# Optimization experiments

Measured on AMD Instinct MI355X. Metric: run time of the kernel, lower is better.

Reference implementation:

```python
import jax, jax.numpy as jnp
import numpy as np

DIM_IN = 512
DIM_OUT = 64


def setup_inputs() -> dict:
    key = jax.random.key(0)
    kx, kq, kk, kv = jax.random.split(key, 4)
    x = jax.random.normal(kx, (4, 4096, DIM_IN), dtype=jnp.float32)
    s = 1.0 / np.sqrt(DIM_IN)
    # torch nn.Linear stores weight as [out, in]; keep same convention
    Wq = jax.random.uniform(kq, (DIM_OUT, DIM_IN), jnp.float32, -s, s)
    Wk = jax.random.uniform(kk, (DIM_OUT, DIM_IN), jnp.float32, -s, s)
    Wv = jax.random.uniform(kv, (DIM_OUT, DIM_IN), jnp.float32, -s, s)
    return {"x": x, "Wq": Wq, "Wk": Wk, "Wv": Wv}


def reference(x, Wq, Wk, Wv):
    # q/k/v projections: [B,S,Din] @ [Din,Dout] -> [B,S,Dout]
    q = jnp.einsum("bsd,od->bso", x, Wq)
    k = jnp.einsum("bsd,od->bso", x, Wk)
    v = jnp.einsum("bsd,od->bso", x, Wv)
    scale = 1.0 / jnp.sqrt(jnp.asarray(q.shape[-1], q.dtype))
    scores = jnp.einsum("bqo,bko->bqk", q, k) * scale  # [B,S,S]
    weights = jax.nn.softmax(scores, axis=-1)
    out = jnp.einsum("bqk,bko->bqo", weights, v)  # [B,S,Dout]
    return out
```

## Files before the change

### kernel.cpp

```cpp
#include <hip/hip_runtime.h>
#include <hip/hip_bf16.h>

#define SEQ 4096
#define MTOT 16384

typedef float f32x4  __attribute__((ext_vector_type(4)));
typedef float f32x16 __attribute__((ext_vector_type(16)));
typedef _Float16 f16;
typedef _Float16 f16x4 __attribute__((ext_vector_type(4)));
typedef _Float16 f16x8 __attribute__((ext_vector_type(8)));
typedef unsigned int   u32;
typedef unsigned int   u32x2 __attribute__((ext_vector_type(2)));
typedef unsigned short u16;

static constexpr size_t QL_B   = 0;
static constexpr size_t KL_B   = 2u << 20;
static constexpr size_t VL_B   = 4u << 20;
static constexpr size_t WL_B   = 6u << 20;

__device__ __forceinline__ u16 h16(float v) { return __builtin_bit_cast(u16, (f16)v); }
__device__ __forceinline__ u32 pkrtz(float a, float b) {
  return __builtin_bit_cast(u32, __builtin_amdgcn_cvt_pkrtz(a, b));
}
__device__ __forceinline__ float ex2(float x) { return __builtin_amdgcn_exp2f(x); }
__device__ __forceinline__ void gl16(const u16* g, u16* l) {
  __builtin_amdgcn_global_load_lds((const __attribute__((address_space(1))) void*)g,
                                   (__attribute__((address_space(3))) void*)l, 16, 0, 0);
}

__global__ __launch_bounds__(256) void wconv_kernel(const float* __restrict__ Wq,
                                                    const float* __restrict__ Wk,
                                                    const float* __restrict__ Wv,
                                                    u16* __restrict__ wlin) {
  const float QSC = 0.18033688011112042f;
  int e = blockIdx.x * 256 + threadIdx.x;
  int flat = e * 4;
  int colg = flat >> 9;
  int k0   = flat & 511;
  int mat  = colg >> 6;
  const float* W = (mat == 0) ? Wq : (mat == 1 ? Wk : Wv);
  f32x4 v = *(const f32x4*)(W + (size_t)(colg & 63) * 512 + k0);
  if (mat == 0) v *= QSC;
  int s = colg >> 4, r16 = colg & 15;
  int step = k0 >> 5, g = (k0 & 31) >> 3, jb = k0 & 7;
  __attribute__((aligned(8))) u16 b[4];
#pragma unroll
  for (int j = 0; j < 4; ++j) b[j] = h16(v[j]);
  *(uint2*)(wlin + ((size_t)(s * 16 + step) * 64 + g * 16 + r16) * 8 + jb) = *(uint2*)b;
}

__global__ __launch_bounds__(256, 4) void proj_kernel(const float* __restrict__ x,
                                                      const u16* __restrict__ wlin,
                                                      u16* __restrict__ ws) {
  __shared__ __attribute__((aligned(16))) u16 xl[8192];
  float* scr = (float*)xl;

  const int tid  = threadIdx.x;
  const int blk  = blockIdx.x;
  const int lane = tid & 63;
  const int ng   = tid >> 6;
  const int r16  = lane & 15;
  const int g    = lane >> 4;
  const int m0   = blk * 16;

#pragma unroll
  for (int i = 0; i < 8; ++i) {
    int f = tid * 4 + i * 1024;
    int row = f >> 9, k0 = f & 511;
    f32x4 v = *(const f32x4*)(x + (size_t)m0 * 512 + f);
    __attribute__((aligned(8))) u16 b[4];
#pragma unroll
    for (int j = 0; j < 4; ++j) b[j] = h16(v[j]);
    int ln = ((k0 & 31) >> 3) * 16 + row;
    *(uint2*)(xl + ((size_t)(k0 >> 5) * 64 + ln) * 8 + (k0 & 7)) = *(uint2*)b;
  }
  __syncthreads();

  f32x4 acc[3];
#pragma unroll
  for (int s = 0; s < 3; ++s) acc[s] = (f32x4){0.f, 0.f, 0.f, 0.f};

#pragma unroll 2
  for (int step = 0; step < 16; ++step) {
    f16x8 a = *(const f16x8*)(xl + ((size_t)step * 64 + lane) * 8);
#pragma unroll
    for (int s = 0; s < 3; ++s) {
      int sg = ng * 3 + s;
      f16x8 b = *(const f16x8*)(wlin + ((size_t)(sg * 16 + step) * 64 + lane) * 8);
      acc[s] = __builtin_amdgcn_mfma_f32_16x16x32_f16(a, b, acc[s], 0, 0, 0);
    }
  }
  __syncthreads();

#pragma unroll
  for (int s = 0; s < 3; ++s)
#pragma unroll
    for (int rr = 0; rr < 4; ++rr)
      scr[(g * 4 + rr) * 193 + ng * 48 + s * 16 + r16] = acc[s][rr];
  __syncthreads();

  u16* Ql = ws + (QL_B >> 1);
  u16* Kl = ws + (KL_B >> 1);
  u16* Vl = ws + (VL_B >> 1);
  const int batch = m0 >> 12;
  const int tile  = (m0 >> 5) & 127;
  const int half  = (m0 >> 4) & 1;

  {
    int t2 = tid & 127;
    int r  = t2 & 15, hh = (t2 >> 4) & 1, ch = t2 >> 5;
    int l31 = half * 16 + r;
    __attribute__((aligned(16))) u16 b[8];
    if (tid < 128) {
#pragma unroll
      for (int j = 0; j < 8; ++j) b[j] = h16(scr[r * 193 + 64 + ch * 16 + hh * 8 + j]);
      *(uint4*)(Kl + ((size_t)((batch * 128 + tile) * 4 + ch) * 64 + hh * 32 + l31) * 8) =
          *(uint4*)b;
    } else {
#pragma unroll
      for (int j = 0; j < 8; ++j) b[j] = h16(scr[r * 193 + ch * 16 + hh * 8 + j]);
      int qhalf = (m0 >> 5);
      *(uint4*)(Ql + ((size_t)(qhalf * 4 + ch) * 64 + hh * 32 + l31) * 8) = *(uint4*)b;
    }
  }
  {
    int z = tid & 1, l31 = (tid >> 1) & 31, hh = (tid >> 6) & 1, db = tid >> 7;
    int d = db * 32 + l31;
    __attribute__((aligned(8))) u16 b[4];
#pragma unroll
    for (int j = 0; j < 4; ++j) b[j] = h16(scr[(8 * z + 4 * hh + j) * 193 + 128 + d]);
    *(uint2*)(Vl + ((size_t)(((batch * 128 + tile) * 2 + db) * 2 + half) * 64 + hh * 32 + l31) *
                       8 + z * 4) = *(uint2*)b;
  }
}

__global__ __launch_bounds__(256, 2) void attn_kernel(const u16* __restrict__ ws,
                                                      float* __restrict__ out) {
  __shared__ __attribute__((aligned(16))) u16 kvb[4][2][4096];

  const int tid  = threadIdx.x;
  const int w    = tid >> 6;
  const int lane = tid & 63;
  const int l31  = lane & 31;
  const int h    = lane >> 5;
  const int bx   = blockIdx.x;
  const int qb   = (bx & 7) * 64 + (bx >> 3);
  const int bb   = qb >> 7;

  const u16* Ql = ws + (QL_B >> 1);
  const u16* Kl = ws + (KL_B >> 1);
  const u16* Vl = ws + (VL_B >> 1);

  f16x8 qf[4];
#pragma unroll
  for (int ch = 0; ch < 4; ++ch)
    qf[ch] = *(const f16x8*)(Ql + ((size_t)(qb * 4 + ch) * 64 + lane) * 8);

  f32x16 oacc[2];
#pragma unroll
  for (int db = 0; db < 2; ++db)
#pragma unroll
    for (int r = 0; r < 16; ++r) oacc[db][r] = 0.f;
  float mrun = -INFINITY, lrun = 0.f;
  const float RTHR = 11.0f;

  const int t0 = bb * 128 + w * 32;
  u16* b0 = &kvb[w][0][0];
  u16* b1 = &kvb[w][1][0];

  auto stage = [&](u16* buf, int t) {
    const u16* ks = Kl + (size_t)t * 2048;
    const u16* vs = Vl + (size_t)t * 2048;
#pragma unroll
    for (int c = 0; c < 4; ++c) gl16(ks + c * 512 + lane * 8, buf + c * 512);
#pragma unroll
    for (int c = 0; c < 4; ++c) gl16(vs + c * 512 + lane * 8, buf + 2048 + c * 512);
  };

  stage(b0, t0);

#pragma unroll 1
  for (int it = 0; it < 32; ++it) {
    u16* cb = (it & 1) ? b1 : b0;
    u16* nb = (it & 1) ? b0 : b1;
    if (it < 31) {
      stage(nb, t0 + it + 1);
      asm volatile("s_waitcnt vmcnt(8)" ::: "memory");
    } else {
      asm volatile("s_waitcnt vmcnt(0)" ::: "memory");
    }
    __builtin_amdgcn_sched_barrier(0);

    f16x8 ka[4], vp[2][2];
#pragma unroll
    for (int ch = 0; ch < 4; ++ch)
      ka[ch] = *(const f16x8*)(cb + (ch * 64 + lane) * 8);
#pragma unroll
    for (int db = 0; db < 2; ++db)
#pragma unroll
      for (int pp = 0; pp < 2; ++pp)
        vp[db][pp] = *(const f16x8*)(cb + 2048 + ((db * 2 + pp) * 64 + lane) * 8);

    f32x16 sac;
#pragma unroll
    for (int r = 0; r < 16; ++r) sac[r] = 0.f;
#pragma unroll
    for (int ch = 0; ch < 4; ++ch)
      sac = __builtin_amdgcn_mfma_f32_32x32x16_f16(ka[ch], qf[ch], sac, 0, 0, 0);

    float mt = sac[0];
#pragma unroll
    for (int r = 1; r < 16; ++r) mt = fmaxf(mt, sac[r]);
    if (__any(mt > mrun + RTHR)) {
      float mtw  = fmaxf(mt, __shfl_xor(mt, 32));
      float nm   = fmaxf(mrun, mtw);
      float corr = ex2(mrun - nm);
      lrun *= corr;
      mrun = nm;
#pragma unroll
      for (int db = 0; db < 2; ++db)
#pragma unroll
        for (int r = 0; r < 16; ++r) oacc[db][r] *= corr;
    }
#pragma unroll
    for (int r = 0; r < 16; ++r) {
      float pv = ex2(sac[r] - mrun);
      sac[r] = pv;
      lrun += pv;
    }

    f16x4 pb[4];
#pragma unroll
    for (int c = 0; c < 4; ++c) {
      u32x2 pk;
      pk[0] = pkrtz(sac[4 * c + 0], sac[4 * c + 1]);
      pk[1] = pkrtz(sac[4 * c + 2], sac[4 * c + 3]);
      pb[c] = __builtin_bit_cast(f16x4, pk);
    }

#pragma unroll
    for (int db = 0; db < 2; ++db)
#pragma unroll
      for (int pp = 0; pp < 2; ++pp) {
        f16x4 vlo = __builtin_shufflevector(vp[db][pp], vp[db][pp], 0, 1, 2, 3);
        f16x4 vhi = __builtin_shufflevector(vp[db][pp], vp[db][pp], 4, 5, 6, 7);
        oacc[db] = __builtin_amdgcn_mfma_f32_32x32x8f16(vlo, pb[2 * pp], oacc[db], 0, 0, 0);
        oacc[db] = __builtin_amdgcn_mfma_f32_32x32x8f16(vhi, pb[2 * pp + 1], oacc[db], 0, 0, 0);
      }
  }

  lrun += __shfl_xor(lrun, 32);

  __syncthreads();
  float* po  = (float*)&kvb[0][0][0];
  float* mls = (float*)((char*)&kvb[0][0][0] + 35840);
  if (h == 0) {
    mls[(w * 32 + l31) * 2 + 0] = mrun;
    mls[(w * 32 + l31) * 2 + 1] = lrun;
  }
  __syncthreads();

  float mg = -INFINITY;
#pragma unroll
  for (int ww = 0; ww < 4; ++ww) mg = fmaxf(mg, mls[(ww * 32 + l31) * 2]);
  float wgt = ex2(mrun - mg);
#pragma unroll
  for (int db = 0; db < 2; ++db)
#pragma unroll
    for (int g = 0; g < 4; ++g) {
      f32x4 v = {oacc[db][4 * g + 0] * wgt, oacc[db][4 * g + 1] * wgt,
                 oacc[db][4 * g + 2] * wgt, oacc[db][4 * g + 3] * wgt};
      *(f32x4*)(po + (size_t)(w * 32 + l31) * 68 + db * 32 + 8 * g + 4 * h) = v;
    }
  __syncthreads();

#pragma unroll
  for (int i = 0; i < 2; ++i) {
    int idx = tid + i * 256;
    int q = idx >> 4, c4 = (idx & 15) * 4;
    float m2 = -INFINITY;
#pragma unroll
    for (int ww = 0; ww < 4; ++ww) m2 = fmaxf(m2, mls[(ww * 32 + q) * 2]);
    float l2 = 0.f;
#pragma unroll
    for (int ww = 0; ww < 4; ++ww)
      l2 += mls[(ww * 32 + q) * 2 + 1] * ex2(mls[(ww * 32 + q) * 2] - m2);
    f32x4 s = (f32x4){0.f, 0.f, 0.f, 0.f};
#pragma unroll
    for (int ww = 0; ww < 4; ++ww) s += *(const f32x4*)(po + (size_t)(ww * 32 + q) * 68 + c4);
    s *= (1.f / l2);
    *(f32x4*)(out + (size_t)(qb * 32 + q) * 64 + c4) = s;
  }
}

extern "C" void kernel_launch(void* const* d_in, const int* in_sizes, int n_in,
                              void* d_out, int out_size, void* d_ws, size_t ws_size,
                              hipStream_t stream) {
  const float* x  = (const float*)d_in[0];
  const float* Wq = (const float*)d_in[1];
  const float* Wk = (const float*)d_in[2];
  const float* Wv = (const float*)d_in[3];
  u16* ws = (u16*)d_ws;
  (void)in_sizes; (void)n_in; (void)out_size; (void)ws_size;

  wconv_kernel<<<96, 256, 0, stream>>>(Wq, Wk, Wv, ws + (WL_B >> 1));
  proj_kernel<<<1024, 256, 0, stream>>>(x, ws + (WL_B >> 1), ws);
  attn_kernel<<<512, 256, 0, stream>>>(ws, (float*)d_out);
}
```

Baseline: 55.03 us.

## Use 512-thread blocks with two query groups; load V directly to registers

Attention blocks grow to 8 waves covering two 32-row query groups that share the same key-split assignment, and the grid halves to 256 blocks. Only K is staged through LDS via async loads; V tiles are now loaded straight from global memory into registers with double buffering. The row max and row sum use tree reductions instead of serial chains. The aim is to cut LDS traffic and footprint and to shorten dependency chains, at the cost of more vector registers and a serialized two-pass final reduction with extra barriers.

```diff
diff --git a/kernel.cpp b/kernel.cpp
--- a/kernel.cpp
+++ b/kernel.cpp
@@ -134,18 +134,20 @@
   }
 }
 
-__global__ __launch_bounds__(256, 2) void attn_kernel(const u16* __restrict__ ws,
+__global__ __launch_bounds__(512, 2) void attn_kernel(const u16* __restrict__ ws,
                                                       float* __restrict__ out) {
-  __shared__ __attribute__((aligned(16))) u16 kvb[4][2][4096];
+  __shared__ __attribute__((aligned(16))) u16 kb[8][2][2048];
 
   const int tid  = threadIdx.x;
   const int w    = tid >> 6;
   const int lane = tid & 63;
   const int l31  = lane & 31;
   const int h    = lane >> 5;
+  const int qg   = w >> 2;
+  const int kq   = w & 3;
   const int bx   = blockIdx.x;
-  const int qb   = (bx & 7) * 64 + (bx >> 3);
-  const int bb   = qb >> 7;
+  const int qb   = (bx & 7) * 32 + (bx >> 3);
+  const int bb   = qb >> 6;
 
   const u16* Ql = ws + (QL_B >> 1);
   const u16* Kl = ws + (KL_B >> 1);
@@ -154,7 +156,7 @@
   f16x8 qf[4];
 #pragma unroll
   for (int ch = 0; ch < 4; ++ch)
-    qf[ch] = *(const f16x8*)(Ql + ((size_t)(qb * 4 + ch) * 64 + lane) * 8);
+    qf[ch] = *(const f16x8*)(Ql + ((size_t)((qb * 2 + qg) * 4 + ch) * 64 + lane) * 8);
 
   f32x16 oacc[2];
 #pragma unroll
@@ -164,42 +166,37 @@
   float mrun = -INFINITY, lrun = 0.f;
   const float RTHR = 11.0f;
 
-  const int t0 = bb * 128 + w * 32;
-  u16* b0 = &kvb[w][0][0];
-  u16* b1 = &kvb[w][1][0];
-
-  auto stage = [&](u16* buf, int t) {
+  const int t0 = bb * 128 + kq * 32;
+  u16* b0 = &kb[w][0][0];
+  u16* b1 = &kb[w][1][0];
+
+  auto stageK = [&](u16* buf, int t) {
     const u16* ks = Kl + (size_t)t * 2048;
-    const u16* vs = Vl + (size_t)t * 2048;
 #pragma unroll
     for (int c = 0; c < 4; ++c) gl16(ks + c * 512 + lane * 8, buf + c * 512);
-#pragma unroll
-    for (int c = 0; c < 4; ++c) gl16(vs + c * 512 + lane * 8, buf + 2048 + c * 512);
   };
-
-  stage(b0, t0);
-
-#pragma unroll 1
-  for (int it = 0; it < 32; ++it) {
-    u16* cb = (it & 1) ? b1 : b0;
-    u16* nb = (it & 1) ? b0 : b1;
-    if (it < 31) {
-      stage(nb, t0 + it + 1);
+  f16x8 v0[2][2], v1[2][2];
+  auto loadV = [&](f16x8(&vv)[2][2], int t) {
+#pragma unroll
+    for (int db = 0; db < 2; ++db)
+#pragma unroll
+      for (int pp = 0; pp < 2; ++pp)
+        vv[db][pp] = *(const f16x8*)(Vl + (size_t)t * 2048 + ((db * 2 + pp) * 64 + lane) * 8);
+  };
+
+  auto body = [&](u16* cb, u16* nb, f16x8(&vc)[2][2], f16x8(&vn)[2][2], int t, bool last) {
+    if (!last) {
+      stageK(nb, t + 1);
+      loadV(vn, t + 1);
       asm volatile("s_waitcnt vmcnt(8)" ::: "memory");
     } else {
       asm volatile("s_waitcnt vmcnt(0)" ::: "memory");
     }
     __builtin_amdgcn_sched_barrier(0);
 
-    f16x8 ka[4], vp[2][2];
-#pragma unroll
-    for (int ch = 0; ch < 4; ++ch)
-      ka[ch] = *(const f16x8*)(cb + (ch * 64 + lane) * 8);
-#pragma unroll
-    for (int db = 0; db < 2; ++db)
-#pragma unroll
-      for (int pp = 0; pp < 2; ++pp)
-        vp[db][pp] = *(const f16x8*)(cb + 2048 + ((db * 2 + pp) * 64 + lane) * 8);
+    f16x8 ka[4];
+#pragma unroll
+    for (int ch = 0; ch < 4; ++ch) ka[ch] = *(const f16x8*)(cb + (ch * 64 + lane) * 8);
 
     f32x16 sac;
 #pragma unroll
@@ -208,9 +205,12 @@
     for (int ch = 0; ch < 4; ++ch)
       sac = __builtin_amdgcn_mfma_f32_32x32x16_f16(ka[ch], qf[ch], sac, 0, 0, 0);
 
-    float mt = sac[0];
-#pragma unroll
-    for (int r = 1; r < 16; ++r) mt = fmaxf(mt, sac[r]);
+    float t8[8];
+#pragma unroll
+    for (int r = 0; r < 8; ++r) t8[r] = fmaxf(sac[2 * r], sac[2 * r + 1]);
+    float t4a = fmaxf(t8[0], t8[1]), t4b = fmaxf(t8[2], t8[3]);
+    float t4c = fmaxf(t8[4], t8[5]), t4d = fmaxf(t8[6], t8[7]);
+    float mt = fmaxf(fmaxf(t4a, t4b), fmaxf(t4c, t4d));
     if (__any(mt > mrun + RTHR)) {
       float mtw  = fmaxf(mt, __shfl_xor(mt, 32));
       float nm   = fmaxf(mrun, mtw);
@@ -223,11 +223,12 @@
         for (int r = 0; r < 16; ++r) oacc[db][r] *= corr;
     }
 #pragma unroll
-    for (int r = 0; r < 16; ++r) {
-      float pv = ex2(sac[r] - mrun);
-      sac[r] = pv;
-      lrun += pv;
-    }
+    for (int r = 0; r < 16; ++r) sac[r] = ex2(sac[r] - mrun);
+    float s4[4];
+#pragma unroll
+    for (int r = 0; r < 4; ++r)
+      s4[r] = (sac[4 * r] + sac[4 * r + 1]) + (sac[4 * r + 2] + sac[4 * r + 3]);
+    lrun += (s4[0] + s4[1]) + (s4[2] + s4[3]);
 
     f16x4 pb[4];
 #pragma unroll
@@ -242,54 +243,65 @@
     for (int db = 0; db < 2; ++db)
 #pragma unroll
       for (int pp = 0; pp < 2; ++pp) {
-        f16x4 vlo = __builtin_shufflevector(vp[db][pp], vp[db][pp], 0, 1, 2, 3);
-        f16x4 vhi = __builtin_shufflevector(vp[db][pp], vp[db][pp], 4, 5, 6, 7);
+        f16x4 vlo = __builtin_shufflevector(vc[db][pp], vc[db][pp], 0, 1, 2, 3);
+        f16x4 vhi = __builtin_shufflevector(vc[db][pp], vc[db][pp], 4, 5, 6, 7);
         oacc[db] = __builtin_amdgcn_mfma_f32_32x32x8f16(vlo, pb[2 * pp], oacc[db], 0, 0, 0);
         oacc[db] = __builtin_amdgcn_mfma_f32_32x32x8f16(vhi, pb[2 * pp + 1], oacc[db], 0, 0, 0);
       }
+  };
+
+  stageK(b0, t0);
+  loadV(v0, t0);
+#pragma unroll 1
+  for (int p = 0; p < 16; ++p) {
+    body(b0, b1, v0, v1, t0 + 2 * p, false);
+    body(b1, b0, v1, v0, t0 + 2 * p + 1, p == 15);
   }
 
   lrun += __shfl_xor(lrun, 32);
 
   __syncthreads();
-  float* po  = (float*)&kvb[0][0][0];
-  float* mls = (float*)((char*)&kvb[0][0][0] + 35840);
+  float* po  = (float*)&kb[0][0][0];
+  float* mls = (float*)((char*)&kb[0][0][0] + 36864);
   if (h == 0) {
     mls[(w * 32 + l31) * 2 + 0] = mrun;
     mls[(w * 32 + l31) * 2 + 1] = lrun;
   }
   __syncthreads();
 
-  float mg = -INFINITY;
-#pragma unroll
-  for (int ww = 0; ww < 4; ++ww) mg = fmaxf(mg, mls[(ww * 32 + l31) * 2]);
-  float wgt = ex2(mrun - mg);
-#pragma unroll
-  for (int db = 0; db < 2; ++db)
-#pragma unroll
-    for (int g = 0; g < 4; ++g) {
-      f32x4 v = {oacc[db][4 * g + 0] * wgt, oacc[db][4 * g + 1] * wgt,
-                 oacc[db][4 * g + 2] * wgt, oacc[db][4 * g + 3] * wgt};
-      *(f32x4*)(po + (size_t)(w * 32 + l31) * 68 + db * 32 + 8 * g + 4 * h) = v;
-    }
-  __syncthreads();
-
-#pragma unroll
-  for (int i = 0; i < 2; ++i) {
-    int idx = tid + i * 256;
-    int q = idx >> 4, c4 = (idx & 15) * 4;
-    float m2 = -INFINITY;
-#pragma unroll
-    for (int ww = 0; ww < 4; ++ww) m2 = fmaxf(m2, mls[(ww * 32 + q) * 2]);
-    float l2 = 0.f;
-#pragma unroll
-    for (int ww = 0; ww < 4; ++ww)
-      l2 += mls[(ww * 32 + q) * 2 + 1] * ex2(mls[(ww * 32 + q) * 2] - m2);
-    f32x4 s = (f32x4){0.f, 0.f, 0.f, 0.f};
-#pragma unroll
-    for (int ww = 0; ww < 4; ++ww) s += *(const f32x4*)(po + (size_t)(ww * 32 + q) * 68 + c4);
-    s *= (1.f / l2);
-    *(f32x4*)(out + (size_t)(qb * 32 + q) * 64 + c4) = s;
+#pragma unroll 1
+  for (int g = 0; g < 2; ++g) {
+    if (qg == g) {
+      float mg = -INFINITY;
+#pragma unroll
+      for (int k2 = 0; k2 < 4; ++k2) mg = fmaxf(mg, mls[((g * 4 + k2) * 32 + l31) * 2]);
+      float wgt = ex2(mrun - mg);
+#pragma unroll
+      for (int db = 0; db < 2; ++db)
+#pragma unroll
+        for (int gg = 0; gg < 4; ++gg) {
+          f32x4 v = {oacc[db][4 * gg + 0] * wgt, oacc[db][4 * gg + 1] * wgt,
+                     oacc[db][4 * gg + 2] * wgt, oacc[db][4 * gg + 3] * wgt};
+          *(f32x4*)(po + (size_t)(kq * 32 + l31) * 68 + db * 32 + 8 * gg + 4 * h) = v;
+        }
+    }
+    __syncthreads();
+    {
+      int q = tid >> 4, c4 = (tid & 15) * 4;
+      float m2 = -INFINITY;
+#pragma unroll
+      for (int k2 = 0; k2 < 4; ++k2) m2 = fmaxf(m2, mls[((g * 4 + k2) * 32 + q) * 2]);
+      float l2 = 0.f;
+#pragma unroll
+      for (int k2 = 0; k2 < 4; ++k2)
+        l2 += mls[((g * 4 + k2) * 32 + q) * 2 + 1] * ex2(mls[((g * 4 + k2) * 32 + q) * 2] - m2);
+      f32x4 s = (f32x4){0.f, 0.f, 0.f, 0.f};
+#pragma unroll
+      for (int k2 = 0; k2 < 4; ++k2) s += *(const f32x4*)(po + (size_t)(k2 * 32 + q) * 68 + c4);
+      s *= (1.f / l2);
+      *(f32x4*)(out + (size_t)(qb * 64 + g * 32 + q) * 64 + c4) = s;
+    }
+    __syncthreads();
   }
 }
 
@@ -305,5 +317,5 @@
 
   wconv_kernel<<<96, 256, 0, stream>>>(Wq, Wk, Wv, ws + (WL_B >> 1));
   proj_kernel<<<1024, 256, 0, stream>>>(x, ws + (WL_B >> 1), ws);
-  attn_kernel<<<512, 256, 0, stream>>>(ws, (float*)d_out);
-}
+  attn_kernel<<<256, 512, 0, stream>>>(ws, (float*)d_out);
+}
```

New measurement: 54.50 us, median of 3. About the same (-1.0%).

## Process two K/V tiles per iteration, load V to registers, sum rows via MFMA

Applied to the files above, without the earlier changes.

The attention loop now handles two 32-key tiles per iteration. Only K is staged into LDS, while V tiles are prefetched straight into registers and double-buffered. The softmax row sum is now computed by an MFMA against a ones vector, replacing the scalar VALU adds and the cross-half shuffle. This aims to cut per-iteration overhead, LDS traffic and VALU work, at the cost of many more VGPRs, which could hurt occupancy at two waves per SIMD. The scratch offset for the final reduction moves to match the new layout.

```diff
diff --git a/kernel.cpp b/kernel.cpp
--- a/kernel.cpp
+++ b/kernel.cpp
@@ -136,7 +136,7 @@
 
 __global__ __launch_bounds__(256, 2) void attn_kernel(const u16* __restrict__ ws,
                                                       float* __restrict__ out) {
-  __shared__ __attribute__((aligned(16))) u16 kvb[4][2][4096];
+  __shared__ __attribute__((aligned(16))) u16 kb[4][2][4096];
 
   const int tid  = threadIdx.x;
   const int w    = tid >> 6;
@@ -156,104 +156,139 @@
   for (int ch = 0; ch < 4; ++ch)
     qf[ch] = *(const f16x8*)(Ql + ((size_t)(qb * 4 + ch) * 64 + lane) * 8);
 
-  f32x16 oacc[2];
+  f32x16 oacc[2], lacc;
 #pragma unroll
   for (int db = 0; db < 2; ++db)
 #pragma unroll
     for (int r = 0; r < 16; ++r) oacc[db][r] = 0.f;
-  float mrun = -INFINITY, lrun = 0.f;
+#pragma unroll
+  for (int r = 0; r < 16; ++r) lacc[r] = 0.f;
+  float mrun = -INFINITY;
   const float RTHR = 11.0f;
+  const f16x4 ones = {(f16)1.f, (f16)1.f, (f16)1.f, (f16)1.f};
 
   const int t0 = bb * 128 + w * 32;
-  u16* b0 = &kvb[w][0][0];
-  u16* b1 = &kvb[w][1][0];
-
-  auto stage = [&](u16* buf, int t) {
-    const u16* ks = Kl + (size_t)t * 2048;
-    const u16* vs = Vl + (size_t)t * 2048;
-#pragma unroll
-    for (int c = 0; c < 4; ++c) gl16(ks + c * 512 + lane * 8, buf + c * 512);
-#pragma unroll
-    for (int c = 0; c < 4; ++c) gl16(vs + c * 512 + lane * 8, buf + 2048 + c * 512);
+  u16* b0 = &kb[w][0][0];
+  u16* b1 = &kb[w][1][0];
+
+  auto stageK = [&](u16* buf, int t) {
+#pragma unroll
+    for (int u = 0; u < 2; ++u)
+#pragma unroll
+      for (int c = 0; c < 4; ++c)
+        gl16(Kl + (size_t)(t + u) * 2048 + c * 512 + lane * 8, buf + u * 2048 + c * 512);
   };
-
-  stage(b0, t0);
-
-#pragma unroll 1
-  for (int it = 0; it < 32; ++it) {
-    u16* cb = (it & 1) ? b1 : b0;
-    u16* nb = (it & 1) ? b0 : b1;
-    if (it < 31) {
-      stage(nb, t0 + it + 1);
-      asm volatile("s_waitcnt vmcnt(8)" ::: "memory");
+  f16x8 vA[2][2][2], vB[2][2][2];
+  auto loadV = [&](f16x8(&vv)[2][2][2], int t) {
+#pragma unroll
+    for (int u = 0; u < 2; ++u)
+#pragma unroll
+      for (int db = 0; db < 2; ++db)
+#pragma unroll
+        for (int pp = 0; pp < 2; ++pp)
+          vv[u][db][pp] =
+              *(const f16x8*)(Vl + (size_t)(t + u) * 2048 + ((db * 2 + pp) * 64 + lane) * 8);
+  };
+
+  auto body = [&](u16* cb, u16* nb, f16x8(&vc)[2][2][2], f16x8(&vn)[2][2][2], int t,
+                  bool last) {
+    if (!last) {
+      stageK(nb, t + 2);
+      loadV(vn, t + 2);
+      asm volatile("s_waitcnt vmcnt(16)" ::: "memory");
     } else {
       asm volatile("s_waitcnt vmcnt(0)" ::: "memory");
     }
     __builtin_amdgcn_sched_barrier(0);
 
-    f16x8 ka[4], vp[2][2];
+    f32x16 sac0, sac1;
+#pragma unroll
+    for (int r = 0; r < 16; ++r) { sac0[r] = 0.f; sac1[r] = 0.f; }
+    f16x8 ka0[4], ka1[4];
+#pragma unroll
+    for (int ch = 0; ch < 4; ++ch) ka0[ch] = *(const f16x8*)(cb + (ch * 64 + lane) * 8);
 #pragma unroll
     for (int ch = 0; ch < 4; ++ch)
-      ka[ch] = *(const f16x8*)(cb + (ch * 64 + lane) * 8);
-#pragma unroll
-    for (int db = 0; db < 2; ++db)
-#pragma unroll
-      for (int pp = 0; pp < 2; ++pp)
-        vp[db][pp] = *(const f16x8*)(cb + 2048 + ((db * 2 + pp) * 64 + lane) * 8);
-
-    f32x16 sac;
-#pragma unroll
-    for (int r = 0; r < 16; ++r) sac[r] = 0.f;
+      ka1[ch] = *(const f16x8*)(cb + 2048 + (ch * 64 + lane) * 8);
 #pragma unroll
     for (int ch = 0; ch < 4; ++ch)
-      sac = __builtin_amdgcn_mfma_f32_32x32x16_f16(ka[ch], qf[ch], sac, 0, 0, 0);
-
-    float mt = sac[0];
-#pragma unroll
-    for (int r = 1; r < 16; ++r) mt = fmaxf(mt, sac[r]);
+      sac0 = __builtin_amdgcn_mfma_f32_32x32x16_f16(ka0[ch], qf[ch], sac0, 0, 0, 0);
+#pragma unroll
+    for (int ch = 0; ch < 4; ++ch)
+      sac1 = __builtin_amdgcn_mfma_f32_32x32x16_f16(ka1[ch], qf[ch], sac1, 0, 0, 0);
+
+    float t16[16];
+#pragma unroll
+    for (int r = 0; r < 16; ++r) t16[r] = fmaxf(sac0[r], sac1[r]);
+#pragma unroll
+    for (int r = 0; r < 8; ++r) t16[r] = fmaxf(t16[r], t16[r + 8]);
+#pragma unroll
+    for (int r = 0; r < 4; ++r) t16[r] = fmaxf(t16[r], t16[r + 4]);
+    float mt = fmaxf(fmaxf(t16[0], t16[1]), fmaxf(t16[2], t16[3]));
     if (__any(mt > mrun + RTHR)) {
       float mtw  = fmaxf(mt, __shfl_xor(mt, 32));
       float nm   = fmaxf(mrun, mtw);
       float corr = ex2(mrun - nm);
-      lrun *= corr;
       mrun = nm;
 #pragma unroll
       for (int db = 0; db < 2; ++db)
 #pragma unroll
         for (int r = 0; r < 16; ++r) oacc[db][r] *= corr;
-    }
-#pragma unroll
-    for (int r = 0; r < 16; ++r) {
-      float pv = ex2(sac[r] - mrun);
-      sac[r] = pv;
-      lrun += pv;
-    }
-
-    f16x4 pb[4];
+#pragma unroll
+      for (int r = 0; r < 16; ++r) lacc[r] *= corr;
+    }
+#pragma unroll
+    for (int r = 0; r < 16; ++r) sac0[r] = ex2(sac0[r] - mrun);
+#pragma unroll
+    for (int r = 0; r < 16; ++r) sac1[r] = ex2(sac1[r] - mrun);
+
+    f16x4 pb0[4], pb1[4];
 #pragma unroll
     for (int c = 0; c < 4; ++c) {
-      u32x2 pk;
-      pk[0] = pkrtz(sac[4 * c + 0], sac[4 * c + 1]);
-      pk[1] = pkrtz(sac[4 * c + 2], sac[4 * c + 3]);
-      pb[c] = __builtin_bit_cast(f16x4, pk);
-    }
+      u32x2 k0, k1;
+      k0[0] = pkrtz(sac0[4 * c + 0], sac0[4 * c + 1]);
+      k0[1] = pkrtz(sac0[4 * c + 2], sac0[4 * c + 3]);
+      k1[0] = pkrtz(sac1[4 * c + 0], sac1[4 * c + 1]);
+      k1[1] = pkrtz(sac1[4 * c + 2], sac1[4 * c + 3]);
+      pb0[c] = __builtin_bit_cast(f16x4, k0);
+      pb1[c] = __builtin_bit_cast(f16x4, k1);
+    }
+
+#pragma unroll
+    for (int c = 0; c < 4; ++c)
+      lacc = __builtin_amdgcn_mfma_f32_32x32x8f16(ones, pb0[c], lacc, 0, 0, 0);
+#pragma unroll
+    for (int c = 0; c < 4; ++c)
+      lacc = __builtin_amdgcn_mfma_f32_32x32x8f16(ones, pb1[c], lacc, 0, 0, 0);
 
 #pragma unroll
     for (int db = 0; db < 2; ++db)
 #pragma unroll
       for (int pp = 0; pp < 2; ++pp) {
-        f16x4 vlo = __builtin_shufflevector(vp[db][pp], vp[db][pp], 0, 1, 2, 3);
-        f16x4 vhi = __builtin_shufflevector(vp[db][pp], vp[db][pp], 4, 5, 6, 7);
-        oacc[db] = __builtin_amdgcn_mfma_f32_32x32x8f16(vlo, pb[2 * pp], oacc[db], 0, 0, 0);
-        oacc[db] = __builtin_amdgcn_mfma_f32_32x32x8f16(vhi, pb[2 * pp + 1], oacc[db], 0, 0, 0);
+        f16x4 vlo0 = __builtin_shufflevector(vc[0][db][pp], vc[0][db][pp], 0, 1, 2, 3);
+        f16x4 vhi0 = __builtin_shufflevector(vc[0][db][pp], vc[0][db][pp], 4, 5, 6, 7);
+        oacc[db] = __builtin_amdgcn_mfma_f32_32x32x8f16(vlo0, pb0[2 * pp], oacc[db], 0, 0, 0);
+        oacc[db] = __builtin_amdgcn_mfma_f32_32x32x8f16(vhi0, pb0[2 * pp + 1], oacc[db], 0, 0, 0);
+        f16x4 vlo1 = __builtin_shufflevector(vc[1][db][pp], vc[1][db][pp], 0, 1, 2, 3);
+        f16x4 vhi1 = __builtin_shufflevector(vc[1][db][pp], vc[1][db][pp], 4, 5, 6, 7);
+        oacc[db] = __builtin_amdgcn_mfma_f32_32x32x8f16(vlo1, pb1[2 * pp], oacc[db], 0, 0, 0);
+        oacc[db] = __builtin_amdgcn_mfma_f32_32x32x8f16(vhi1, pb1[2 * pp + 1], oacc[db], 0, 0, 0);
       }
-  }
-
-  lrun += __shfl_xor(lrun, 32);
-
-  __syncthreads();
-  float* po  = (float*)&kvb[0][0][0];
-  float* mls = (float*)((char*)&kvb[0][0][0] + 35840);
+  };
+
+  stageK(b0, t0);
+  loadV(vA, t0);
+#pragma unroll 1
+  for (int p = 0; p < 8; ++p) {
+    body(b0, b1, vA, vB, t0 + 4 * p, false);
+    body(b1, b0, vB, vA, t0 + 4 * p + 2, p == 7);
+  }
+
+  float lrun = lacc[0];
+
+  __syncthreads();
+  float* po  = (float*)&kb[0][0][0];
+  float* mls = (float*)((char*)&kb[0][0][0] + 36864);
   if (h == 0) {
     mls[(w * 32 + l31) * 2 + 0] = mrun;
     mls[(w * 32 + l31) * 2 + 1] = lrun;
```

New measurement: 58.47 us. +6.2%, slower.
